# Optimization experiments

Measured on AMD Instinct MI355X. Metric: run time of the kernel, lower is better.

The kernel has to match this reference:

```python
import jax, jax.numpy as jnp
import numpy as np

N_ATOMS = 50000
IN_DIM = 128
HID = 256
N_ELEM = 4
N_IMG = 500
NNZ = 2_000_000
ELEMENTS = jnp.array([1, 6, 8, 29], dtype=jnp.int64)


def setup_inputs() -> dict:
    key = jax.random.key(0)
    ks = jax.random.split(key, 14)
    fingerprints = jax.random.normal(ks[0], (N_ATOMS, IN_DIM), dtype=jnp.float32)
    # atomic numbers drawn from the supported element set
    elem_idx = jax.random.randint(ks[1], (N_ATOMS,), 0, N_ELEM)
    atomic_numbers = ELEMENTS[elem_idx]
    image_idx = jnp.sort(jax.random.randint(ks[2], (N_ATOMS,), 0, N_IMG))
    # sparse fprimes (COO): [N_ATOMS*IN_DIM, 3*N_ATOMS]
    fprime_rows = jax.random.randint(ks[3], (NNZ,), 0, N_ATOMS * IN_DIM)
    fprime_cols = jax.random.randint(ks[4], (NNZ,), 0, 3 * N_ATOMS)
    fprime_vals = jax.random.normal(ks[5], (NNZ,), dtype=jnp.float32) * 0.1
    # per-element MLP params, stacked over the element axis (torch Linear-style init)
    s0, s1 = 1.0 / np.sqrt(IN_DIM), 1.0 / np.sqrt(HID)
    W0 = jax.random.uniform(ks[6], (N_ELEM, IN_DIM, HID), jnp.float32, -s0, s0)
    b0 = jax.random.uniform(ks[7], (N_ELEM, HID), jnp.float32, -s0, s0)
    W1 = jax.random.uniform(ks[8], (N_ELEM, HID, HID), jnp.float32, -s1, s1)
    b1 = jax.random.uniform(ks[9], (N_ELEM, HID), jnp.float32, -s1, s1)
    W2 = jax.random.uniform(ks[10], (N_ELEM, HID, 1), jnp.float32, -s1, s1)
    b2 = jax.random.uniform(ks[11], (N_ELEM, 1), jnp.float32, -s1, s1)
    return {"fingerprints": fingerprints, "atomic_numbers": atomic_numbers,
            "image_idx": image_idx, "fprime_rows": fprime_rows,
            "fprime_cols": fprime_cols, "fprime_vals": fprime_vals,
            "W0": W0, "b0": b0, "W1": W1, "b1": b1, "W2": W2, "b2": b2}


def _per_atom_energy(fp, atomic_numbers, W0, b0, W1, b1, W2, b2):
    # Run every element-specific MLP over ALL atoms (as the torch module does),
    # then mask by the one-hot element membership and sum over elements.
    h = jnp.tanh(jnp.einsum('nd,edh->enh', fp, W0) + b0[:, None, :])   # [E,N,H]
    h = jnp.tanh(jnp.einsum('enh,ehk->enk', h, W1) + b1[:, None, :])   # [E,N,H]
    out = jnp.einsum('enh,eho->eno', h, W2) + b2[:, None, :]           # [E,N,1]
    mask = (atomic_numbers[None, :] == ELEMENTS[:, None]).astype(fp.dtype)  # [E,N]
    return jnp.sum(mask * out[..., 0], axis=0)                          # [N]


def reference(fingerprints, atomic_numbers, image_idx, fprime_rows,
              fprime_cols, fprime_vals, W0, b0, W1, b1, W2, b2):
    o = _per_atom_energy(fingerprints, atomic_numbers, W0, b0, W1, b1, W2, b2)
    energy = jax.ops.segment_sum(o, image_idx, num_segments=N_IMG)  # [N_IMG]
    # dE/dfp for forces (sum over images == sum over atoms of o)
    g = jax.grad(lambda fp: jnp.sum(
        _per_atom_energy(fp, atomic_numbers, W0, b0, W1, b1, W2, b2)))(fingerprints)
    g_flat = g.reshape(-1)  # [N*D]
    # forces = -fprimes^T @ g_flat, fprimes in COO form
    forces = -jax.ops.segment_sum(fprime_vals * g_flat[fprime_rows],
                                  fprime_cols, num_segments=3 * N_ATOMS)
    return energy, forces.reshape(N_ATOMS, 3)
```

## Files before the change

### kernel.cpp

```cpp
#include <hip/hip_runtime.h>
#include <math.h>

#define N_ATOMS 50000
#define IN_DIM 128
#define HID 256
#define N_ELEM 4
#define N_IMG 500
#define NNZ 2000000

#define CBINS 293
#define CW 512
#define BCAP 8192
#define OCAP 4096
#define PCH 3008
#define NBP ((NNZ + PCH - 1) / PCH)
#define TILES_PER_E 416
#define NFB (8 * (TILES_PER_E / 2))
#define TOTB (NBP + NFB)
#define BKB ((N_ATOMS + 255) / 256)
#define PREPB 384

typedef __attribute__((ext_vector_type(8))) short bf16x8;
typedef __attribute__((ext_vector_type(4))) float f32x4;
typedef __attribute__((ext_vector_type(4))) int   i32x4;
typedef __attribute__((ext_vector_type(4))) float fv4;

__device__ __forceinline__ int elem_of(int z) {
    return (z == 1) ? 0 : (z == 6) ? 1 : (z == 8) ? 2 : 3;
}

__device__ __forceinline__ unsigned short f2bf(float f) {
    unsigned u = __float_as_uint(f);
    u += 0x7fffu + ((u >> 16) & 1u);
    return (unsigned short)(u >> 16);
}
__device__ __forceinline__ float bf2f(unsigned short u) {
    return __uint_as_float(((unsigned)u) << 16);
}
__device__ __forceinline__ float tanh_fast(float x) {
    float e = __expf(2.f * x);
    return (e - 1.f) / (e + 1.f);
}

__global__ __launch_bounds__(256) void prep_and_bucket(
    const float* __restrict__ W0, const float* __restrict__ W1,
    unsigned short* __restrict__ W0s1,
    unsigned short* __restrict__ W1s2,
    unsigned short* __restrict__ W1s3,
    unsigned short* __restrict__ W0s4,
    const int* __restrict__ Z, int* __restrict__ counts,
    int* __restrict__ lists, float* __restrict__ F) {

    const int tid = threadIdx.x;

    if (blockIdx.x >= PREPB) {
        __shared__ int lcnt[N_ELEM], lbase[N_ELEM];
        const int bb = blockIdx.x - PREPB;
        for (int idx = bb * 256 + tid; idx < 3 * N_ATOMS; idx += BKB * 256)
            F[idx] = 0.f;
        const int i = bb * 256 + tid;
        if (tid < N_ELEM) lcnt[tid] = 0;
        __syncthreads();
        int e = -1, pos = 0;
        if (i < N_ATOMS) {
            e = elem_of(Z[i]);
            pos = atomicAdd(&lcnt[e], 1);
        }
        __syncthreads();
        if (tid < N_ELEM) lbase[tid] = atomicAdd(&counts[tid], lcnt[tid]);
        __syncthreads();
        if (i < N_ATOMS) lists[e * N_ATOMS + lbase[e] + pos] = i;
        return;
    }

    const int T = blockIdx.x * 256 + tid;

    if (T < 32768) {
        const int e = T >> 13, fid = T & 8191;
        const int blkv = fid >> 6, lane = fid & 63;
        const int k0 = ((blkv & 7) << 5) | ((lane >> 4) << 3);
        const int n  = ((blkv >> 3) << 4) | (lane & 15);
        const float* src = W1 + e * 65536 + n;
        bf16x8 vv;
#pragma unroll
        for (int j = 0; j < 8; ++j) vv[j] = (short)f2bf(src[(k0 + j) * 256]);
        *(bf16x8*)(W1s2 + (e << 16) + (fid << 3)) = vv;
    } else if (T < 65536) {
        const int u = T - 32768, e = u >> 13, fid = u & 8191;
        const int blkv = fid >> 6, lane = fid & 63;
        const int k  = ((blkv >> 3) << 4) | (lane & 15);
        const int n0 = ((blkv & 7) << 5) | ((lane >> 4) << 3);
        const float* src = W1 + e * 65536 + k * 256 + n0;
        float4 a = *(const float4*)src;
        float4 b = *(const float4*)(src + 4);
        bf16x8 vv;
        vv[0] = (short)f2bf(a.x); vv[1] = (short)f2bf(a.y);
        vv[2] = (short)f2bf(a.z); vv[3] = (short)f2bf(a.w);
        vv[4] = (short)f2bf(b.x); vv[5] = (short)f2bf(b.y);
        vv[6] = (short)f2bf(b.z); vv[7] = (short)f2bf(b.w);
        *(bf16x8*)(W1s3 + (e << 16) + (fid << 3)) = vv;
    } else if (T < 81920) {
        const int u = T - 65536, e = u >> 12, fid = u & 4095;
        const int blkv = fid >> 6, lane = fid & 63;
        const int k0 = ((blkv & 3) << 5) | ((lane >> 4) << 3);
        const int n  = ((blkv >> 2) << 4) | (lane & 15);
        const float* src = W0 + e * 32768 + n;
        bf16x8 vv;
#pragma unroll
        for (int j = 0; j < 8; ++j) vv[j] = (short)f2bf(src[(k0 + j) * 256]);
        *(bf16x8*)(W0s1 + e * 32768 + (fid << 3)) = vv;
    } else if (T < 98304) {
        const int u = T - 81920, e = u >> 12, fid = u & 4095;
        const int blkv = fid >> 6, lane = fid & 63;
        const int k  = ((blkv >> 3) << 4) | (lane & 15);
        const int n0 = ((blkv & 7) << 5) | ((lane >> 4) << 3);
        const float* src = W0 + e * 32768 + k * 256 + n0;
        float4 a = *(const float4*)src;
        float4 b = *(const float4*)(src + 4);
        bf16x8 vv;
        vv[0] = (short)f2bf(a.x); vv[1] = (short)f2bf(a.y);
        vv[2] = (short)f2bf(a.z); vv[3] = (short)f2bf(a.w);
        vv[4] = (short)f2bf(b.x); vv[5] = (short)f2bf(b.y);
        vv[6] = (short)f2bf(b.z); vv[7] = (short)f2bf(b.w);
        *(bf16x8*)(W0s4 + e * 32768 + (fid << 3)) = vv;
    }
}

#define CH 1280
__global__ __launch_bounds__(256, 4) void mega_mlp_bin(
    const float* __restrict__ fp,
    const unsigned short* __restrict__ W0s1,
    const unsigned short* __restrict__ W1s2,
    const unsigned short* __restrict__ W1s3,
    const unsigned short* __restrict__ W0s4,
    const float* __restrict__ b0, const float* __restrict__ b1,
    const float* __restrict__ W2, const float* __restrict__ b2,
    float* __restrict__ o_atom,
    unsigned short* __restrict__ Gb,
    const int* __restrict__ counts, const int* __restrict__ lists,
    const int* __restrict__ rows, const int* __restrict__ cols,
    const float* __restrict__ vals,
    unsigned* __restrict__ pvB,
    int* __restrict__ gcur,
    int* __restrict__ ovfR, int* __restrict__ ovfC, float* __restrict__ ovfV,
    int* __restrict__ ocur) {

    __shared__ __align__(16) char smem[40960];
    const int tid = threadIdx.x;

    const int bid = blockIdx.x;
    const int pA = (bid * NBP) / TOTB;
    const int pB = ((bid + 1) * NBP) / TOTB;

    if (pB > pA) {
        int*   Lr    = (int*)smem;
        int*   Lc    = (int*)(smem + 12032);
        float* Lv    = (float*)(smem + 24064);
        int*   hist  = (int*)(smem + 36096);
        int*   pref  = (int*)(smem + 37268);
        int*   curs  = (int*)(smem + 38440);
        int*   gbase = (int*)(smem + 39612);

        const int base = pA * PCH;
        const int lim = (base + PCH <= NNZ) ? PCH : (NNZ - base);

        for (int i = tid; i < CBINS; i += 256) hist[i] = 0;
        __syncthreads();

        i32x4 r[3], c[3];
        fv4   v[3];
        int nvalid[3];
#pragma unroll
        for (int j = 0; j < 3; ++j) {
            const int li = tid * 4 + 1024 * j;
            const int i0 = base + li;
            int nv = lim - li;
            nvalid[j] = nv > 4 ? 4 : (nv < 0 ? 0 : nv);
            if (nvalid[j] == 4) {
                r[j] = __builtin_nontemporal_load((const i32x4*)(rows + i0));
                c[j] = __builtin_nontemporal_load((const i32x4*)(cols + i0));
                v[j] = __builtin_nontemporal_load((const fv4*)(vals + i0));
            } else {
                for (int e2 = 0; e2 < nvalid[j]; ++e2) {
                    r[j][e2] = rows[i0 + e2]; c[j][e2] = cols[i0 + e2];
                    v[j][e2] = vals[i0 + e2];
                }
            }
#pragma unroll
            for (int e2 = 0; e2 < 4; ++e2)
                if (e2 < nvalid[j]) atomicAdd(&hist[c[j][e2] >> 9], 1);
        }
        __syncthreads();

        if (tid < 64) {
            int carry = 0;
#pragma unroll
            for (int cch = 0; cch < 5; ++cch) {
                const int i = cch * 64 + tid;
                const int h = (i < CBINS) ? hist[i] : 0;
                int x = h;
#pragma unroll
                for (int off = 1; off < 64; off <<= 1) {
                    int y = __shfl_up(x, off, 64);
                    if (tid >= off) x += y;
                }
                if (i < CBINS) pref[i] = carry + x - h;
                carry += __shfl(x, 63, 64);
            }
        }
        __syncthreads();
        for (int b = tid; b < CBINS; b += 256) {
            gbase[b] = atomicAdd(&gcur[b], hist[b]);
            curs[b] = pref[b];
        }
        __syncthreads();

#pragma unroll
        for (int j = 0; j < 3; ++j)
#pragma unroll
            for (int e2 = 0; e2 < 4; ++e2)
                if (e2 < nvalid[j]) {
                    int b = c[j][e2] >> 9;
                    int p = atomicAdd(&curs[b], 1);
                    Lr[p] = r[j][e2]; Lc[p] = c[j][e2]; Lv[p] = v[j][e2];
                }
        __syncthreads();

#pragma unroll
        for (int j = 0; j < 12; ++j) {
            const int p = tid + 256 * j;
            if (p >= lim) break;
            const int col = Lc[p];
            const int b = col >> 9;
            const int g = gbase[b] + (p - pref[b]);
            if (g < BCAP) {
                uint2 w;
                w.x = ((unsigned)(col & 511) << 23) | (unsigned)Lr[p];
                w.y = __float_as_uint(Lv[p]);
                *(uint2*)(pvB + (((size_t)b * BCAP + g) << 1)) = w;
            } else {
                int od = atomicAdd(ocur, 1);
                if (od < OCAP) { ovfR[od] = Lr[p]; ovfC[od] = col; ovfV[od] = Lv[p]; }
            }
        }
        return;
    }

    const int fid = bid - pB;
    const int xcd = fid & 7;
    const int e = xcd & 3;
    const int tile = (fid >> 3) * 2 + (xcd >> 2);
    const int cnt = counts[e];
    const int m0 = tile * 32;
    if (m0 >= cnt) return;
    const int* list = lists + e * N_ATOMS;

    short* tH = (short*)smem;
    short* tD = (short*)(smem + 20480);

    const int lane = tid & 63;
    const int wv = tid >> 6;
    const int lr = lane & 15;
    const int lq = lane >> 4;

    const unsigned short* B1 = W0s1 + (size_t)e * HID * IN_DIM;
    const unsigned short* B2 = W1s2 + (size_t)e * HID * HID;
    const unsigned short* B3 = W1s3 + (size_t)e * HID * HID;
    const unsigned short* B4 = W0s4 + (size_t)e * IN_DIM * HID;

    f32x4 acc[2][4];
#define ZERO_ACC()                                                        \
    _Pragma("unroll") for (int mt = 0; mt < 2; ++mt)                      \
        _Pragma("unroll") for (int nt = 0; nt < 4; ++nt)                  \
            _Pragma("unroll") for (int j = 0; j < 4; ++j) acc[mt][nt][j] = 0.f;

    {
        bf16x8 bb0[4];
#pragma unroll
        for (int nt = 0; nt < 4; ++nt)
            bb0[nt] = *(const bf16x8*)(B1 +
                ((size_t)(((wv * 4 + nt) * 4 + 0) * 64 + lane) << 3));

#pragma unroll
        for (int p = 0; p < 4; ++p) {
            const int row = p * 8 + (tid >> 5);
            const int col = (tid & 31) * 4;
            const int m = m0 + row;
            float4 a = make_float4(0.f, 0.f, 0.f, 0.f);
            if (m < cnt)
                a = *(const float4*)(fp + (size_t)list[m] * IN_DIM + col);
            short4 b;
            b.x = (short)f2bf(a.x); b.y = (short)f2bf(a.y);
            b.z = (short)f2bf(a.z); b.w = (short)f2bf(a.w);
            *(short4*)&tD[(col >> 5) * CH + row * 40 + (col & 31)] = b;
        }
        __syncthreads();

        ZERO_ACC();
        bf16x8 bb[2][4];
#pragma unroll
        for (int nt = 0; nt < 4; ++nt) bb[0][nt] = bb0[nt];
#pragma unroll
        for (int ki = 0; ki < 4; ++ki) {
            const int cur = ki & 1, nx = cur ^ 1;
            if (ki < 3) {
#pragma unroll
                for (int nt = 0; nt < 4; ++nt)
                    bb[nx][nt] = *(const bf16x8*)(B1 +
                        ((size_t)(((wv * 4 + nt) * 4 + ki + 1) * 64 + lane) << 3));
            }
            bf16x8 af[2];
#pragma unroll
            for (int mt = 0; mt < 2; ++mt)
                af[mt] = *(const bf16x8*)&tD[ki * CH + (mt * 16 + lr) * 40 + lq * 8];
#pragma unroll
            for (int mt = 0; mt < 2; ++mt)
#pragma unroll
                for (int nt = 0; nt < 4; ++nt)
                    acc[mt][nt] = __builtin_amdgcn_mfma_f32_16x16x32_bf16(
                        af[mt], bb[cur][nt], acc[mt][nt], 0, 0, 0);
        }
    }

    bf16x8 b2r[3][4];
#pragma unroll
    for (int p = 0; p < 3; ++p)
#pragma unroll
        for (int nt = 0; nt < 4; ++nt)
            b2r[p][nt] = *(const bf16x8*)(B2 +
                ((size_t)(((wv * 4 + nt) * 8 + p) * 64 + lane) << 3));

    {
        float bv[4];
#pragma unroll
        for (int nt = 0; nt < 4; ++nt)
            bv[nt] = b0[e * HID + wv * 64 + nt * 16 + lr];
#pragma unroll
        for (int mt = 0; mt < 2; ++mt)
#pragma unroll
            for (int rr = 0; rr < 4; ++rr) {
                const int row = mt * 16 + lq * 4 + rr;
#pragma unroll
                for (int nt = 0; nt < 4; ++nt) {
                    const int n = wv * 64 + nt * 16 + lr;
                    float t = tanh_fast(acc[mt][nt][rr] + bv[nt]);
                    tH[(n >> 5) * CH + row * 40 + (n & 31)] = (short)f2bf(t);
                }
            }
    }
    __syncthreads();

    ZERO_ACC();
#pragma unroll
    for (int ki = 0; ki < 8; ++ki) {
        bf16x8 af[2];
#pragma unroll
        for (int mt = 0; mt < 2; ++mt)
            af[mt] = *(const bf16x8*)&tH[ki * CH + (mt * 16 + lr) * 40 + lq * 8];
#pragma unroll
        for (int mt = 0; mt < 2; ++mt)
#pragma unroll
            for (int nt = 0; nt < 4; ++nt)
                acc[mt][nt] = __builtin_amdgcn_mfma_f32_16x16x32_bf16(
                    af[mt], b2r[ki % 3][nt], acc[mt][nt], 0, 0, 0);
        if (ki < 5) {
#pragma unroll
            for (int nt = 0; nt < 4; ++nt)
                b2r[ki % 3][nt] = *(const bf16x8*)(B2 +
                    ((size_t)(((wv * 4 + nt) * 8 + ki + 3) * 64 + lane) << 3));
        }
    }

    bf16x8 b3r[3][4];
#pragma unroll
    for (int p = 0; p < 3; ++p)
#pragma unroll
        for (int nt = 0; nt < 4; ++nt)
            b3r[p][nt] = *(const bf16x8*)(B3 +
                ((size_t)(((wv * 4 + nt) * 8 + p) * 64 + lane) << 3));

    {
        float bv[4], w2v[4];
#pragma unroll
        for (int nt = 0; nt < 4; ++nt) {
            bv[nt]  = b1[e * HID + wv * 64 + nt * 16 + lr];
            w2v[nt] = W2[e * HID + wv * 64 + nt * 16 + lr];
        }
#pragma unroll
        for (int mt = 0; mt < 2; ++mt)
#pragma unroll
            for (int rr = 0; rr < 4; ++rr) {
                const int row = mt * 16 + lq * 4 + rr;
                float osum = 0.f;
#pragma unroll
                for (int nt = 0; nt < 4; ++nt) {
                    const int n = wv * 64 + nt * 16 + lr;
                    float t = tanh_fast(acc[mt][nt][rr] + bv[nt]);
                    osum += t * w2v[nt];
                    tD[(n >> 5) * CH + row * 40 + (n & 31)] =
                        (short)f2bf(w2v[nt] * (1.f - t * t));
                }
                osum += __shfl_xor(osum, 1, 64);
                osum += __shfl_xor(osum, 2, 64);
                osum += __shfl_xor(osum, 4, 64);
                osum += __shfl_xor(osum, 8, 64);
                if (lr == 0)
                    ((float*)&tD[row * 40 + 32])[wv] = osum;
            }
    }
    __syncthreads();
    if (tid < 32) {
        int m = m0 + tid;
        if (m < cnt) {
            const float4 r4 = *(const float4*)&tD[tid * 40 + 32];
            o_atom[list[m]] = r4.x + r4.y + r4.z + r4.w + b2[e];
        }
    }

    ZERO_ACC();
#pragma unroll
    for (int ki = 0; ki < 8; ++ki) {
        bf16x8 af[2];
#pragma unroll
        for (int mt = 0; mt < 2; ++mt)
            af[mt] = *(const bf16x8*)&tD[ki * CH + (mt * 16 + lr) * 40 + lq * 8];
#pragma unroll
        for (int mt = 0; mt < 2; ++mt)
#pragma unroll
            for (int nt = 0; nt < 4; ++nt)
                acc[mt][nt] = __builtin_amdgcn_mfma_f32_16x16x32_bf16(
                    af[mt], b3r[ki % 3][nt], acc[mt][nt], 0, 0, 0);
        if (ki < 5) {
#pragma unroll
            for (int nt = 0; nt < 4; ++nt)
                b3r[ki % 3][nt] = *(const bf16x8*)(B3 +
                    ((size_t)(((wv * 4 + nt) * 8 + ki + 3) * 64 + lane) << 3));
        }
    }

    bf16x8 b4r[3][2];
#pragma unroll
    for (int p = 0; p < 3; ++p)
#pragma unroll
        for (int nt = 0; nt < 2; ++nt)
            b4r[p][nt] = *(const bf16x8*)(B4 +
                ((size_t)(((wv * 2 + nt) * 8 + p) * 64 + lane) << 3));

#pragma unroll
    for (int mt = 0; mt < 2; ++mt)
#pragma unroll
        for (int rr = 0; rr < 4; ++rr) {
            const int row = mt * 16 + lq * 4 + rr;
#pragma unroll
            for (int nt = 0; nt < 4; ++nt) {
                const int n = wv * 64 + nt * 16 + lr;
                const int a = (n >> 5) * CH + row * 40 + (n & 31);
                float h = bf2f((unsigned short)tH[a]);
                tH[a] = (short)f2bf(acc[mt][nt][rr] * (1.f - h * h));
            }
        }
    __syncthreads();

    {
        f32x4 a4[2][2];
#pragma unroll
        for (int mt = 0; mt < 2; ++mt)
#pragma unroll
            for (int nt = 0; nt < 2; ++nt)
#pragma unroll
                for (int j = 0; j < 4; ++j) a4[mt][nt][j] = 0.f;
#pragma unroll
        for (int ki = 0; ki < 8; ++ki) {
            bf16x8 af[2];
#pragma unroll
            for (int mt = 0; mt < 2; ++mt)
                af[mt] = *(const bf16x8*)&tH[ki * CH + (mt * 16 + lr) * 40 + lq * 8];
#pragma unroll
            for (int mt = 0; mt < 2; ++mt)
#pragma unroll
                for (int nt = 0; nt < 2; ++nt)
                    a4[mt][nt] = __builtin_amdgcn_mfma_f32_16x16x32_bf16(
                        af[mt], b4r[ki % 3][nt], a4[mt][nt], 0, 0, 0);
            if (ki < 5) {
#pragma unroll
                for (int nt = 0; nt < 2; ++nt)
                    b4r[ki % 3][nt] = *(const bf16x8*)(B4 +
                        ((size_t)(((wv * 2 + nt) * 8 + ki + 3) * 64 + lane) << 3));
            }
        }
#pragma unroll
        for (int mt = 0; mt < 2; ++mt)
#pragma unroll
            for (int rr = 0; rr < 4; ++rr) {
                const int row = mt * 16 + lq * 4 + rr;
#pragma unroll
                for (int nt = 0; nt < 2; ++nt) {
                    const int n = wv * 32 + nt * 16 + lr;
                    tD[(n >> 5) * CH + row * 40 + (n & 31)] =
                        (short)f2bf(a4[mt][nt][rr]);
                }
            }
    }
    __syncthreads();
#pragma unroll
    for (int t = 0; t < 2; ++t) {
        const int c = tid + 256 * t;
        const int row = c >> 4;
        const int pos = (c & 15) * 8;
        const int m = m0 + row;
        if (m < cnt) {
            bf16x8 v = *(const bf16x8*)&tD[(pos >> 5) * CH + row * 40 + (pos & 31)];
            *(bf16x8*)(Gb + (size_t)list[m] * IN_DIM + pos) = v;
        }
    }
#undef ZERO_ACC
}

__global__ __launch_bounds__(1024) void forces_consumer(
    const unsigned* __restrict__ pvB,
    const int* __restrict__ gcur,
    const unsigned short* __restrict__ g, float* __restrict__ F,
    const float* __restrict__ o_atom, const int* __restrict__ img,
    float* __restrict__ energy,
    const int* __restrict__ ovfR, const int* __restrict__ ovfC,
    const float* __restrict__ ovfV, const int* __restrict__ ocur) {

    const int blk = blockIdx.x;
    const int tid = threadIdx.x;

    if (blk < CBINS) {
        __shared__ float win[CW];
        for (int i = tid; i < CW; i += 1024) win[i] = 0.f;
        __syncthreads();
        const int w0 = blk << 9;
        int cnt = gcur[blk]; if (cnt > BCAP) cnt = BCAP;
        const unsigned* base = pvB + (((size_t)blk * BCAP) << 1);
        const int i0 = tid * 8;
        if (i0 < cnt) {
            if (i0 + 8 <= cnt) {
                const i32x4* src = (const i32x4*)(base + (i0 << 1));
                i32x4 q0 = __builtin_nontemporal_load(src);
                i32x4 q1 = __builtin_nontemporal_load(src + 1);
                i32x4 q2 = __builtin_nontemporal_load(src + 2);
                i32x4 q3 = __builtin_nontemporal_load(src + 3);
                unsigned pk[8]; float vv[8];
                pk[0] = (unsigned)q0[0]; vv[0] = __uint_as_float(q0[1]);
                pk[1] = (unsigned)q0[2]; vv[1] = __uint_as_float(q0[3]);
                pk[2] = (unsigned)q1[0]; vv[2] = __uint_as_float(q1[1]);
                pk[3] = (unsigned)q1[2]; vv[3] = __uint_as_float(q1[3]);
                pk[4] = (unsigned)q2[0]; vv[4] = __uint_as_float(q2[1]);
                pk[5] = (unsigned)q2[2]; vv[5] = __uint_as_float(q2[3]);
                pk[6] = (unsigned)q3[0]; vv[6] = __uint_as_float(q3[1]);
                pk[7] = (unsigned)q3[2]; vv[7] = __uint_as_float(q3[3]);
                float gv[8];
#pragma unroll
                for (int j = 0; j < 8; ++j)
                    gv[j] = bf2f(g[pk[j] & 0x7FFFFFu]);
#pragma unroll
                for (int j = 0; j < 8; ++j)
                    atomicAdd(&win[pk[j] >> 23], -vv[j] * gv[j]);
            } else {
                for (int e2 = i0; e2 < cnt; ++e2) {
                    unsigned pk = base[e2 << 1];
                    float vv = __uint_as_float(base[(e2 << 1) + 1]);
                    atomicAdd(&win[pk >> 23], -vv * bf2f(g[pk & 0x7FFFFFu]));
                }
            }
        }
        {
            int ocnt = ocur[0]; if (ocnt > OCAP) ocnt = OCAP;
            for (int k2 = tid; k2 < ocnt; k2 += 1024) {
                int c = ovfC[k2];
                if (c >= w0 && c < w0 + CW)
                    atomicAdd(&win[c - w0], -ovfV[k2] * bf2f(g[ovfR[k2]]));
            }
        }
        __syncthreads();
        for (int i = tid; i < CW; i += 1024) {
            int c = w0 + i;
            if (c < 3 * N_ATOMS) F[c] = win[i];
        }
        return;
    }

    {
        const int bb = blk - CBINS;
        int lo, hi;
        {
            int l = 0, r = N_ATOMS;
            while (l < r) { int m = (l + r) >> 1; if (img[m] < bb) l = m + 1; else r = m; }
            lo = l;
        }
        {
            int l = lo, r = N_ATOMS;
            while (l < r) { int m = (l + r) >> 1; if (img[m] < bb + 1) l = m + 1; else r = m; }
            hi = l;
        }
        float s = 0.f;
        for (int i2 = lo + tid; i2 < hi; i2 += 1024) s += o_atom[i2];
#pragma unroll
        for (int off = 32; off > 0; off >>= 1) s += __shfl_down(s, off, 64);
        __shared__ float red[16];
        if ((tid & 63) == 0) red[tid >> 6] = s;
        __syncthreads();
        if (tid == 0) {
            float t = 0.f;
#pragma unroll
            for (int w2 = 0; w2 < 16; ++w2) t += red[w2];
            energy[bb] = t;
        }
    }
}

extern "C" void kernel_launch(void* const* d_in, const int* in_sizes, int n_in,
                              void* d_out, int out_size, void* d_ws, size_t ws_size,
                              hipStream_t stream) {
    const float* fp    = (const float*)d_in[0];
    const int*   Z     = (const int*)d_in[1];
    const int*   img   = (const int*)d_in[2];
    const int*   frows = (const int*)d_in[3];
    const int*   fcols = (const int*)d_in[4];
    const float* fvals = (const float*)d_in[5];
    const float* W0    = (const float*)d_in[6];
    const float* b0    = (const float*)d_in[7];
    const float* W1    = (const float*)d_in[8];
    const float* b1    = (const float*)d_in[9];
    const float* W2    = (const float*)d_in[10];
    const float* b2    = (const float*)d_in[11];

    float* out    = (float*)d_out;
    float* energy = out;
    float* F      = out + N_IMG;

    char* ws = (char*)d_ws;
    int*   counts = (int*)ws;
    int*   gcur   = (int*)(ws + 32);
    int*   ocur   = (int*)(ws + 32 + 4 * CBINS);
    int*   lists  = (int*)(ws + 4096);
    char*  base   = ws + (1 << 20);
    unsigned short* Gb   = (unsigned short*)(base);
    float* o_atom        = (float*)(base + 13000000);
    unsigned short* W0s1 = (unsigned short*)(base + 14000000);
    unsigned short* W0s4 = W0s1 + N_ELEM * IN_DIM * HID;
    unsigned short* W1s2 = W0s4 + N_ELEM * IN_DIM * HID;
    unsigned short* W1s3 = W1s2 + N_ELEM * HID * HID;
    unsigned* pvB = (unsigned*)(base + 19000000);
    int*   ovfR  = (int*)(base + 49000000);
    int*   ovfC  = (int*)(base + 49050000);
    float* ovfV  = (float*)(base + 49100000);

    hipMemsetAsync(ws, 0, 32 + 4 * CBINS + 4, stream);

    prep_and_bucket<<<PREPB + BKB, 256, 0, stream>>>(
        W0, W1, W0s1, W1s2, W1s3, W0s4, Z, counts, lists, F);

    mega_mlp_bin<<<TOTB, 256, 0, stream>>>(
        fp, W0s1, W1s2, W1s3, W0s4, b0, b1, W2, b2, o_atom, Gb, counts, lists,
        frows, fcols, fvals, pvB, gcur, ovfR, ovfC, ovfV, ocur);

    forces_consumer<<<CBINS + N_IMG, 1024, 0, stream>>>(
        pvB, gcur, Gb, F, o_atom, img, energy,
        ovfR, ovfC, ovfV, ocur);
}
```

Measured before the change: 193.9 us.

## Replace padded LDS tiles with XOR swizzle to shrink shared memory and raise occupancy

Drops the 40-element row padding in the MLP LDS tiles in favour of an XOR swizzle, which cuts shared memory from 40KB to 32KB and allows 5 blocks per CU instead of 4. The binning chunk size is reduced to fit the smaller buffer, so more binning blocks are launched. The per-row energy partial sums now stay in registers and are written to LDS later, after the final GEMM stage, because the padding slot that held them no longer exists. The risks are extra register pressure from the held sums and swizzle patterns that may not remove every bank conflict.

```diff
diff --git a/kernel.cpp b/kernel.cpp
--- a/kernel.cpp
+++ b/kernel.cpp
@@ -12,13 +12,15 @@
 #define CW 512
 #define BCAP 8192
 #define OCAP 4096
-#define PCH 3008
+#define PCH 2304
 #define NBP ((NNZ + PCH - 1) / PCH)
 #define TILES_PER_E 416
 #define NFB (8 * (TILES_PER_E / 2))
 #define TOTB (NBP + NFB)
 #define BKB ((N_ATOMS + 255) / 256)
 #define PREPB 384
+
+#define SWZ(row, col) ((col) ^ ((((row) >> 2) & 3) << 3))
 
 typedef __attribute__((ext_vector_type(8))) short bf16x8;
 typedef __attribute__((ext_vector_type(4))) float f32x4;
@@ -126,8 +128,8 @@
     }
 }
 
-#define CH 1280
-__global__ __launch_bounds__(256, 4) void mega_mlp_bin(
+#define CH 1024
+__global__ __launch_bounds__(256, 5) void mega_mlp_bin(
     const float* __restrict__ fp,
     const unsigned short* __restrict__ W0s1,
     const unsigned short* __restrict__ W1s2,
@@ -145,7 +147,7 @@
     int* __restrict__ ovfR, int* __restrict__ ovfC, float* __restrict__ ovfV,
     int* __restrict__ ocur) {
 
-    __shared__ __align__(16) char smem[40960];
+    __shared__ __align__(16) char smem[32768];
     const int tid = threadIdx.x;
 
     const int bid = blockIdx.x;
@@ -154,12 +156,12 @@
 
     if (pB > pA) {
         int*   Lr    = (int*)smem;
-        int*   Lc    = (int*)(smem + 12032);
-        float* Lv    = (float*)(smem + 24064);
-        int*   hist  = (int*)(smem + 36096);
-        int*   pref  = (int*)(smem + 37268);
-        int*   curs  = (int*)(smem + 38440);
-        int*   gbase = (int*)(smem + 39612);
+        int*   Lc    = (int*)(smem + 9216);
+        float* Lv    = (float*)(smem + 18432);
+        int*   hist  = (int*)(smem + 27648);
+        int*   pref  = (int*)(smem + 28820);
+        int*   curs  = (int*)(smem + 29992);
+        int*   gbase = (int*)(smem + 31164);
 
         const int base = pA * PCH;
         const int lim = (base + PCH <= NNZ) ? PCH : (NNZ - base);
@@ -227,7 +229,7 @@
         __syncthreads();
 
 #pragma unroll
-        for (int j = 0; j < 12; ++j) {
+        for (int j = 0; j < 9; ++j) {
             const int p = tid + 256 * j;
             if (p >= lim) break;
             const int col = Lc[p];
@@ -256,12 +258,13 @@
     const int* list = lists + e * N_ATOMS;
 
     short* tH = (short*)smem;
-    short* tD = (short*)(smem + 20480);
+    short* tD = (short*)(smem + 16384);
 
     const int lane = tid & 63;
     const int wv = tid >> 6;
     const int lr = lane & 15;
     const int lq = lane >> 4;
+    const int fsw = ((lr >> 2) & 3) << 3;
 
     const unsigned short* B1 = W0s1 + (size_t)e * HID * IN_DIM;
     const unsigned short* B2 = W1s2 + (size_t)e * HID * HID;
@@ -269,6 +272,7 @@
     const unsigned short* B4 = W0s4 + (size_t)e * IN_DIM * HID;
 
     f32x4 acc[2][4];
+    float osumR[2][4];
 #define ZERO_ACC()                                                        \
     _Pragma("unroll") for (int mt = 0; mt < 2; ++mt)                      \
         _Pragma("unroll") for (int nt = 0; nt < 4; ++nt)                  \
@@ -292,7 +296,7 @@
             short4 b;
             b.x = (short)f2bf(a.x); b.y = (short)f2bf(a.y);
             b.z = (short)f2bf(a.z); b.w = (short)f2bf(a.w);
-            *(short4*)&tD[(col >> 5) * CH + row * 40 + (col & 31)] = b;
+            *(short4*)&tD[(col >> 5) * CH + row * 32 + SWZ(row, col & 31)] = b;
         }
         __syncthreads();
 
@@ -312,7 +316,7 @@
             bf16x8 af[2];
 #pragma unroll
             for (int mt = 0; mt < 2; ++mt)
-                af[mt] = *(const bf16x8*)&tD[ki * CH + (mt * 16 + lr) * 40 + lq * 8];
+                af[mt] = *(const bf16x8*)&tD[ki * CH + (mt * 16 + lr) * 32 + (lq * 8 ^ fsw)];
 #pragma unroll
             for (int mt = 0; mt < 2; ++mt)
 #pragma unroll
@@ -344,7 +348,7 @@
                 for (int nt = 0; nt < 4; ++nt) {
                     const int n = wv * 64 + nt * 16 + lr;
                     float t = tanh_fast(acc[mt][nt][rr] + bv[nt]);
-                    tH[(n >> 5) * CH + row * 40 + (n & 31)] = (short)f2bf(t);
+                    tH[(n >> 5) * CH + row * 32 + SWZ(row, n & 31)] = (short)f2bf(t);
                 }
             }
     }
@@ -356,7 +360,7 @@
         bf16x8 af[2];
 #pragma unroll
         for (int mt = 0; mt < 2; ++mt)
-            af[mt] = *(const bf16x8*)&tH[ki * CH + (mt * 16 + lr) * 40 + lq * 8];
+            af[mt] = *(const bf16x8*)&tH[ki * CH + (mt * 16 + lr) * 32 + (lq * 8 ^ fsw)];
 #pragma unroll
         for (int mt = 0; mt < 2; ++mt)
 #pragma unroll
@@ -397,25 +401,17 @@
                     const int n = wv * 64 + nt * 16 + lr;
                     float t = tanh_fast(acc[mt][nt][rr] + bv[nt]);
                     osum += t * w2v[nt];
-                    tD[(n >> 5) * CH + row * 40 + (n & 31)] =
+                    tD[(n >> 5) * CH + row * 32 + SWZ(row, n & 31)] =
                         (short)f2bf(w2v[nt] * (1.f - t * t));
                 }
                 osum += __shfl_xor(osum, 1, 64);
                 osum += __shfl_xor(osum, 2, 64);
                 osum += __shfl_xor(osum, 4, 64);
                 osum += __shfl_xor(osum, 8, 64);
-                if (lr == 0)
-                    ((float*)&tD[row * 40 + 32])[wv] = osum;
+                osumR[mt][rr] = osum;
             }
     }
     __syncthreads();
-    if (tid < 32) {
-        int m = m0 + tid;
-        if (m < cnt) {
-            const float4 r4 = *(const float4*)&tD[tid * 40 + 32];
-            o_atom[list[m]] = r4.x + r4.y + r4.z + r4.w + b2[e];
-        }
-    }
 
     ZERO_ACC();
 #pragma unroll
@@ -423,7 +419,7 @@
         bf16x8 af[2];
 #pragma unroll
         for (int mt = 0; mt < 2; ++mt)
-            af[mt] = *(const bf16x8*)&tD[ki * CH + (mt * 16 + lr) * 40 + lq * 8];
+            af[mt] = *(const bf16x8*)&tD[ki * CH + (mt * 16 + lr) * 32 + (lq * 8 ^ fsw)];
 #pragma unroll
         for (int mt = 0; mt < 2; ++mt)
 #pragma unroll
@@ -454,7 +450,7 @@
 #pragma unroll
             for (int nt = 0; nt < 4; ++nt) {
                 const int n = wv * 64 + nt * 16 + lr;
-                const int a = (n >> 5) * CH + row * 40 + (n & 31);
+                const int a = (n >> 5) * CH + row * 32 + SWZ(row, n & 31);
                 float h = bf2f((unsigned short)tH[a]);
                 tH[a] = (short)f2bf(acc[mt][nt][rr] * (1.f - h * h));
             }
@@ -474,7 +470,7 @@
             bf16x8 af[2];
 #pragma unroll
             for (int mt = 0; mt < 2; ++mt)
-                af[mt] = *(const bf16x8*)&tH[ki * CH + (mt * 16 + lr) * 40 + lq * 8];
+                af[mt] = *(const bf16x8*)&tH[ki * CH + (mt * 16 + lr) * 32 + (lq * 8 ^ fsw)];
 #pragma unroll
             for (int mt = 0; mt < 2; ++mt)
 #pragma unroll
@@ -496,9 +492,11 @@
 #pragma unroll
                 for (int nt = 0; nt < 2; ++nt) {
                     const int n = wv * 32 + nt * 16 + lr;
-                    tD[(n >> 5) * CH + row * 40 + (n & 31)] =
+                    tD[(n >> 5) * CH + row * 32 + SWZ(row, n & 31)] =
                         (short)f2bf(a4[mt][nt][rr]);
                 }
+                if (lr == 0)
+                    ((float*)&tD[4 * CH])[wv * 32 + row] = osumR[mt][rr];
             }
     }
     __syncthreads();
@@ -509,8 +507,16 @@
         const int pos = (c & 15) * 8;
         const int m = m0 + row;
         if (m < cnt) {
-            bf16x8 v = *(const bf16x8*)&tD[(pos >> 5) * CH + row * 40 + (pos & 31)];
+            bf16x8 v = *(const bf16x8*)&tD[(pos >> 5) * CH + row * 32 + SWZ(row, pos & 31)];
             *(bf16x8*)(Gb + (size_t)list[m] * IN_DIM + pos) = v;
+        }
+    }
+    if (tid < 32) {
+        int m = m0 + tid;
+        if (m < cnt) {
+            const float* rp = (const float*)&tD[4 * CH];
+            o_atom[list[m]] = rp[tid] + rp[32 + tid] + rp[64 + tid] +
+                              rp[96 + tid] + b2[e];
         }
     }
 #undef ZERO_ACC
```

Measured after the change: 312.6 us. 1.61x slower.
